# Kernel optimization log

Measured on AMD Instinct MI355X. Metric: run time of the kernel, lower is better.

The kernel has to match this reference:

```python
import jax, jax.numpy as jnp
import numpy as np

N = 50000      # nodes
E = 800000     # edges (before self loops)
IN, H, OUT = 128, 64, 64
NEG_SLOPE = 0.2  # PyG GATConv leaky_relu slope


def _glorot(k, shape):
    lim = float(np.sqrt(6.0 / (shape[0] + shape[1])))
    return jax.random.uniform(k, shape, jnp.float32, -lim, lim)


def setup_inputs() -> dict:
    key = jax.random.key(0)
    ks = jax.random.split(key, 16)
    x = jax.random.normal(ks[0], (N, IN), jnp.float32)
    edge_src = jax.random.randint(ks[1], (E,), 0, N, jnp.int32)
    edge_dst = jax.random.randint(ks[2], (E,), 0, N, jnp.int32)
    dims = [(IN, H), (H, H), (H, OUT)]
    inp = {"x": x, "edge_src": edge_src, "edge_dst": edge_dst}
    i = 3
    for l, (di, do) in enumerate(dims):
        inp[f"W{l}"] = _glorot(ks[i], (di, do)); i += 1
        inp[f"as{l}"] = _glorot(ks[i], (1, do))[0]; i += 1
        inp[f"ad{l}"] = _glorot(ks[i], (1, do))[0]; i += 1
        inp[f"b{l}"] = jnp.zeros((do,), jnp.float32)
    return inp


def _gat_layer(x, W, a_src, a_dst, b, src, dst):
    # single-head GATConv (PyG semantics, self loops already in src/dst)
    h = x @ W                              # [N, do]
    s = h @ a_src                          # [N] source attention logits
    d = h @ a_dst                          # [N] dest attention logits
    e = jax.nn.leaky_relu(s[src] + d[dst], NEG_SLOPE)   # [E']
    # segment softmax over incoming edges of each destination node
    m = jax.ops.segment_max(e, dst, num_segments=N)
    w = jnp.exp(e - m[dst])
    denom = jax.ops.segment_sum(w, dst, num_segments=N)
    coef = w / (denom[dst] + 1e-16)
    out = jax.ops.segment_sum(h[src] * coef[:, None], dst, num_segments=N)
    return out + b


def reference(x, edge_src, edge_dst, W0, as0, ad0, b0, W1, as1, ad1, b1, W2, as2, ad2, b2):
    # add self loops (GATConv default add_self_loops=True)
    loop = jnp.arange(N, dtype=edge_src.dtype)
    src = jnp.concatenate([edge_src, loop])
    dst = jnp.concatenate([edge_dst, loop])
    h = jax.nn.relu(_gat_layer(x, W0, as0, ad0, b0, src, dst))
    # dropout is identity in eval mode
    h = jax.nn.relu(_gat_layer(h, W1, as1, ad1, b1, src, dst))
    return _gat_layer(h, W2, as2, ad2, b2, src, dst)
```

## Files before the change

### kernel.cpp

```cpp
#include <hip/hip_runtime.h>
#include <hip/hip_fp16.h>
#include <math.h>

#define WAVE 64
#define NEG_SLOPE 0.2f
#define BCAP 4096
#define CSTR (BCAP + 128)

typedef _Float16 half8 __attribute__((ext_vector_type(8)));
typedef float f32x4 __attribute__((ext_vector_type(4)));


template <int K, int IS_HALF>
__device__ __forceinline__ void gemm_body(
    char* smemRaw, int t, int bid,
    const void* __restrict__ Xv, const float* __restrict__ W,
    const float* __restrict__ a_s, const float* __restrict__ a_d,
    __half* __restrict__ H, float* __restrict__ S, float* __restrict__ D,
    int n) {
    constexpr int AK = K + 8;
    _Float16* Xs = (_Float16*)smemRaw;
    _Float16* Bt = Xs + 64 * AK;
    int base = bid * 64;

    {
        int row = t >> 2, q = t & 3;
        int grow = base + row;
        constexpr int CW = K / 4;
        if constexpr (IS_HALF) {
            const __half* Xh = (const __half*)Xv;
#pragma unroll
            for (int c0 = 0; c0 < CW; c0 += 8) {
                uint4 v = make_uint4(0, 0, 0, 0);
                if (grow < n) v = *(const uint4*)(Xh + (size_t)grow * K + q * CW + c0);
                *(uint4*)(Xs + row * AK + q * CW + c0) = v;
            }
        } else {
            const float* X = (const float*)Xv;
#pragma unroll
            for (int c0 = 0; c0 < CW; c0 += 8) {
                float4 v0 = make_float4(0.f, 0.f, 0.f, 0.f), v1 = v0;
                if (grow < n) {
                    v0 = *(const float4*)(X + (size_t)grow * K + q * CW + c0);
                    v1 = *(const float4*)(X + (size_t)grow * K + q * CW + c0 + 4);
                }
                _Float16 h[8] = {(_Float16)v0.x, (_Float16)v0.y, (_Float16)v0.z, (_Float16)v0.w,
                                 (_Float16)v1.x, (_Float16)v1.y, (_Float16)v1.z, (_Float16)v1.w};
                *(uint4*)(Xs + row * AK + q * CW + c0) = *(uint4*)h;
            }
        }
    }
    {
        int nn = t & 63, g = t >> 6;
        constexpr int KW = K / 4;
        _Float16 hbuf[KW];
#pragma unroll
        for (int j = 0; j < KW; ++j)
            hbuf[j] = (_Float16)W[(size_t)(g * KW + j) * 64 + nn];
#pragma unroll
        for (int j = 0; j < KW; j += 8)
            *(uint4*)(Bt + nn * AK + g * KW + j) = *(uint4*)(hbuf + j);
    }
    __syncthreads();

    int lane = t & 63;
    int wv = t >> 6;
    int m0 = wv * 16;
    int l15 = lane & 15, quad = lane >> 4;

    f32x4 acc[4] = {{0.f, 0.f, 0.f, 0.f}, {0.f, 0.f, 0.f, 0.f},
                    {0.f, 0.f, 0.f, 0.f}, {0.f, 0.f, 0.f, 0.f}};
#pragma unroll
    for (int ks = 0; ks < K; ks += 32) {
        half8 a = *(half8*)(Xs + (m0 + l15) * AK + ks + quad * 8);
#pragma unroll
        for (int cg = 0; cg < 4; ++cg) {
            half8 b = *(half8*)(Bt + (cg * 16 + l15) * AK + ks + quad * 8);
            acc[cg] = __builtin_amdgcn_mfma_f32_16x16x32_f16(a, b, acc[cg], 0, 0, 0);
        }
    }

    float as_c[4], ad_c[4];
#pragma unroll
    for (int cg = 0; cg < 4; ++cg) {
        as_c[cg] = a_s[cg * 16 + l15];
        ad_c[cg] = a_d[cg * 16 + l15];
    }
#pragma unroll
    for (int r = 0; r < 4; ++r) {
        int grow = base + m0 + quad * 4 + r;
        bool ok = grow < n;
        float ps = 0.f, pd = 0.f;
#pragma unroll
        for (int cg = 0; cg < 4; ++cg) {
            float v = acc[cg][r];
            if (ok) H[(size_t)grow * 64 + cg * 16 + l15] = __float2half(v);
            ps += v * as_c[cg];
            pd += v * ad_c[cg];
        }
        for (int o = 1; o < 16; o <<= 1) {
            ps += __shfl_xor(ps, o);
            pd += __shfl_xor(pd, o);
        }
        if (l15 == 0 && ok) { S[grow] = ps; D[grow] = pd; }
    }
}

__global__ __launch_bounds__(256) void place_gemm0_kernel(
    const int* __restrict__ src, const int* __restrict__ dst,
    int* __restrict__ gfill, int* __restrict__ binned, int e, int nb, int nchunk,
    const float* __restrict__ X, const float* __restrict__ W,
    const float* __restrict__ a_s, const float* __restrict__ a_d,
    __half* __restrict__ H, float* __restrict__ S, float* __restrict__ D, int n) {
    extern __shared__ char smem[];
    if ((int)blockIdx.x >= nchunk) {
        gemm_body<128, 0>(smem, threadIdx.x, blockIdx.x - nchunk,
                          X, W, a_s, a_d, H, S, D, n);
        return;
    }
    int* cnt = (int*)smem;
    int* bas = cnt + nb;
    for (int b = threadIdx.x; b < nb; b += 256) cnt[b] = 0;
    __syncthreads();
    int base = blockIdx.x * 4096;
#pragma unroll
    for (int k = 0; k < 16; ++k) {
        int i = base + k * 256 + threadIdx.x;
        if (i < e) atomicAdd(&cnt[dst[i] >> 7], 1);
    }
    __syncthreads();
    for (int b = threadIdx.x; b < nb; b += 256) {
        int c = cnt[b];
        bas[b] = c ? atomicAdd(&gfill[b], c) : 0;
        cnt[b] = 0;
    }
    __syncthreads();
#pragma unroll
    for (int k = 0; k < 16; ++k) {
        int i = base + k * 256 + threadIdx.x;
        if (i < e) {
            int d = dst[i];
            int bk = d >> 7;
            int r = atomicAdd(&cnt[bk], 1);
            binned[(size_t)bk * BCAP + bas[bk] + r] = ((d & 127) << 16) | src[i];
        }
    }
}

__global__ __launch_bounds__(256) void bucket_build_kernel(
    const int* __restrict__ binned, const int* __restrict__ gfill,
    int* __restrict__ csr_src, int2* __restrict__ rowse, int n) {
    __shared__ int cnt[128], off[128], pcnt[128];
    int b = blockIdx.x;
    int t = threadIdx.x;
    int nodeBase = b << 7;
    int nc = min(128, n - nodeBase);
    int ne = min(gfill[b], BCAP);
    const int* bp = binned + (size_t)b * BCAP;
    if (t < 128) { cnt[t] = 1; pcnt[t] = 1; }
    __syncthreads();
    for (int i = t; i < ne; i += 256)
        atomicAdd(&cnt[bp[i] >> 16], 1);
    __syncthreads();
    if (t < 128) off[t] = cnt[t];
    __syncthreads();
    for (int o = 1; o < 128; o <<= 1) {
        int u = (t >= o && t < 128) ? off[t - o] : 0;
        __syncthreads();
        if (t < 128) off[t] += u;
        __syncthreads();
    }
    if (t < 128) off[t] -= cnt[t];
    __syncthreads();
    int csrBase = b * CSTR;
    if (t < nc) {
        int st = csrBase + off[t];
        rowse[nodeBase + t] = make_int2(st, st + cnt[t]);
        csr_src[st] = nodeBase + t;
    }
    for (int i = t; i < ne; i += 256) {
        int p = bp[i];
        int loc = p >> 16;
        int r = atomicAdd(&pcnt[loc], 1);
        csr_src[csrBase + off[loc] + r] = p & 0xFFFF;
    }
}

template <int K, int IS_HALF>
__global__ __launch_bounds__(256) void mfma_gemm_feat_kernel(
    const void* __restrict__ Xv, const float* __restrict__ W,
    const float* __restrict__ a_s, const float* __restrict__ a_d,
    __half* __restrict__ H, float* __restrict__ S, float* __restrict__ D, int n) {
    __shared__ char smem[2 * 64 * (K + 8) * 2];
    gemm_body<K, IS_HALF>(smem, threadIdx.x, blockIdx.x, Xv, W, a_s, a_d, H, S, D, n);
}


template <int WRITE_HALF>
__global__ __launch_bounds__(256) void gat_aggregate_kernel(
    const __half* __restrict__ H, const float* __restrict__ S,
    const float* __restrict__ D, const int2* __restrict__ rowse,
    const int* __restrict__ csr_src, const float* __restrict__ bias,
    void* __restrict__ OUTp, int n, int do_relu) {
    int wid  = (blockIdx.x * blockDim.x + threadIdx.x) >> 6;
    int lane = threadIdx.x & 63;
    if (wid >= n) return;
    int eg = lane >> 3;
    int cg = lane & 7;
    int2 se = rowse[wid];
    int start = se.x, end = se.y;
    float d_i = D[wid];

    float z = 0.f;
    float acc[8] = {0.f, 0.f, 0.f, 0.f, 0.f, 0.f, 0.f, 0.f};

    for (int cb = start; cb < end; cb += WAVE) {
        int j = cb + lane;
        bool v = j < end;
        int sc = v ? csr_src[j] : 0;
        float sv = S[sc];
        float e = sv + d_i;
        e = (e > 0.f) ? e : NEG_SLOPE * e;
        float w = v ? __expf(e) : 0.f;
        z += w;

        int nch = min(WAVE, end - cb);
        int rounds = (nch + 7) >> 3;
#pragma unroll 4
        for (int r = 0; r < rounds; ++r) {
            int idx = 8 * r + eg;
            float wr = __shfl(w, idx);
            int   sr = __shfl(sc, idx);
            if (idx < nch) {
                uint4 u = *(const uint4*)(H + (size_t)sr * 64 + 8 * cg);
                float2 f0 = __half22float2(*(__half2*)&u.x);
                float2 f1 = __half22float2(*(__half2*)&u.y);
                float2 f2 = __half22float2(*(__half2*)&u.z);
                float2 f3 = __half22float2(*(__half2*)&u.w);
                acc[0] = fmaf(wr, f0.x, acc[0]);
                acc[1] = fmaf(wr, f0.y, acc[1]);
                acc[2] = fmaf(wr, f1.x, acc[2]);
                acc[3] = fmaf(wr, f1.y, acc[3]);
                acc[4] = fmaf(wr, f2.x, acc[4]);
                acc[5] = fmaf(wr, f2.y, acc[5]);
                acc[6] = fmaf(wr, f3.x, acc[6]);
                acc[7] = fmaf(wr, f3.y, acc[7]);
            }
        }
    }

    z += __shfl_xor(z, 1);
    z += __shfl_xor(z, 2);
    z += __shfl_xor(z, 4);
    for (int o = 8; o < 64; o <<= 1) {
#pragma unroll
        for (int jj = 0; jj < 8; ++jj) acc[jj] += __shfl_xor(acc[jj], o);
        z += __shfl_xor(z, o);
    }

    if (eg == 0) {
        float inv = 1.f / (z + 1e-16f);
        const float4 bv0 = *(const float4*)(bias + 8 * cg);
        const float4 bv1 = *(const float4*)(bias + 8 * cg + 4);
        float o[8];
        o[0] = acc[0] * inv + bv0.x;
        o[1] = acc[1] * inv + bv0.y;
        o[2] = acc[2] * inv + bv0.z;
        o[3] = acc[3] * inv + bv0.w;
        o[4] = acc[4] * inv + bv1.x;
        o[5] = acc[5] * inv + bv1.y;
        o[6] = acc[6] * inv + bv1.z;
        o[7] = acc[7] * inv + bv1.w;
        if (do_relu) {
#pragma unroll
            for (int jj = 0; jj < 8; ++jj) o[jj] = fmaxf(o[jj], 0.f);
        }
        if constexpr (WRITE_HALF) {
            _Float16 h[8];
#pragma unroll
            for (int jj = 0; jj < 8; ++jj) h[jj] = (_Float16)o[jj];
            *(uint4*)((__half*)OUTp + (size_t)wid * 64 + 8 * cg) = *(uint4*)h;
        } else {
            float* OUT = (float*)OUTp;
            *(float4*)(OUT + (size_t)wid * 64 + 8 * cg) = make_float4(o[0], o[1], o[2], o[3]);
            *(float4*)(OUT + (size_t)wid * 64 + 8 * cg + 4) = make_float4(o[4], o[5], o[6], o[7]);
        }
    }
}


static inline size_t align256(size_t x) { return (x + 255) & ~(size_t)255; }

extern "C" void kernel_launch(void* const* d_in, const int* in_sizes, int n_in,
                              void* d_out, int out_size, void* d_ws, size_t ws_size,
                              hipStream_t stream) {
    const float* x    = (const float*)d_in[0];
    const int*   esrc = (const int*)d_in[1];
    const int*   edst = (const int*)d_in[2];
    const int E = in_sizes[1];
    const int N = in_sizes[0] / 128;

    const float* W0 = (const float*)d_in[3];
    const float* as0 = (const float*)d_in[4];
    const float* ad0 = (const float*)d_in[5];
    const float* b0 = (const float*)d_in[6];
    const float* W1 = (const float*)d_in[7];
    const float* as1 = (const float*)d_in[8];
    const float* ad1 = (const float*)d_in[9];
    const float* b1 = (const float*)d_in[10];
    const float* W2 = (const float*)d_in[11];
    const float* as2 = (const float*)d_in[12];
    const float* ad2 = (const float*)d_in[13];
    const float* b2 = (const float*)d_in[14];

    const int NB = (N + 127) >> 7;

    char* p = (char*)d_ws;
    int*  gfill   = (int*)p;  p += align256((size_t)(NB + 1) * 4);
    int2* rowse   = (int2*)p; p += align256((size_t)N * 8);
    int*  csr_src = (int*)p;  p += align256((size_t)NB * CSTR * 4);
    int*  binned  = (int*)p;  p += align256((size_t)NB * BCAP * 4);
    __half* h16 = (__half*)p; p += align256((size_t)N * 64 * 2);
    __half* hA  = (__half*)p; p += align256((size_t)N * 64 * 2);
    __half* hB  = (__half*)p; p += align256((size_t)N * 64 * 2);
    float* sA = (float*)p; p += align256((size_t)N * 4);
    float* dA = (float*)p; p += align256((size_t)N * 4);
    float* out = (float*)d_out;

    int nchunk = (E + 4095) / 4096;
    int tile_grid = (N + 63) / 64;
    int agg_grid  = (N + 3) / 4;

    hipMemsetAsync(gfill, 0, (size_t)(NB + 1) * 4, stream);

    place_gemm0_kernel<<<nchunk + tile_grid, 256, 34816, stream>>>(
        esrc, edst, gfill, binned, E, NB, nchunk,
        x, W0, as0, ad0, h16, sA, dA, N);

    bucket_build_kernel<<<NB, 256, 0, stream>>>(binned, gfill, csr_src, rowse, N);

    gat_aggregate_kernel<1><<<agg_grid, 256, 0, stream>>>(
        h16, sA, dA, rowse, csr_src, b0, hA, N, 1);

    mfma_gemm_feat_kernel<64, 1><<<tile_grid, 256, 0, stream>>>(hA, W1, as1, ad1, h16, sA, dA, N);
    gat_aggregate_kernel<1><<<agg_grid, 256, 0, stream>>>(
        h16, sA, dA, rowse, csr_src, b1, hB, N, 1);

    mfma_gemm_feat_kernel<64, 1><<<tile_grid, 256, 0, stream>>>(hB, W2, as2, ad2, h16, sA, dA, N);
    gat_aggregate_kernel<0><<<agg_grid, 256, 0, stream>>>(
        h16, sA, dA, rowse, csr_src, b2, out, N, 0);
}
```

Baseline: 235.0 us.

## Fuse GAT aggregation with next layer's MFMA feature GEMM

Replaces the separate aggregate and GEMM kernels for layers 0→1 and 1→2 with a single kernel. Each 512-thread block aggregates 64 nodes into shared memory as fp16, then runs the MFMA projection and the attention-logit reduction on that tile. This removes two kernel launches and the global write and read of the intermediate hidden activations, and adds ping-pong H/S/D buffers. It also widens bucket_build to 512 threads. The cost is that each wave now handles 8 nodes serially, which can lower latency hiding in the gather phase.

```diff
diff --git a/kernel.cpp b/kernel.cpp
--- a/kernel.cpp
+++ b/kernel.cpp
@@ -147,7 +147,7 @@
     }
 }
 
-__global__ __launch_bounds__(256) void bucket_build_kernel(
+__global__ __launch_bounds__(512) void bucket_build_kernel(
     const int* __restrict__ binned, const int* __restrict__ gfill,
     int* __restrict__ csr_src, int2* __restrict__ rowse, int n) {
     __shared__ int cnt[128], off[128], pcnt[128];
@@ -159,7 +159,7 @@
     const int* bp = binned + (size_t)b * BCAP;
     if (t < 128) { cnt[t] = 1; pcnt[t] = 1; }
     __syncthreads();
-    for (int i = t; i < ne; i += 256)
+    for (int i = t; i < ne; i += 512)
         atomicAdd(&cnt[bp[i] >> 16], 1);
     __syncthreads();
     if (t < 128) off[t] = cnt[t];
@@ -178,7 +178,7 @@
         rowse[nodeBase + t] = make_int2(st, st + cnt[t]);
         csr_src[st] = nodeBase + t;
     }
-    for (int i = t; i < ne; i += 256) {
+    for (int i = t; i < ne; i += 512) {
         int p = bp[i];
         int loc = p >> 16;
         int r = atomicAdd(&pcnt[loc], 1);
@@ -186,34 +186,19 @@
     }
 }
 
-template <int K, int IS_HALF>
-__global__ __launch_bounds__(256) void mfma_gemm_feat_kernel(
-    const void* __restrict__ Xv, const float* __restrict__ W,
-    const float* __restrict__ a_s, const float* __restrict__ a_d,
-    __half* __restrict__ H, float* __restrict__ S, float* __restrict__ D, int n) {
-    __shared__ char smem[2 * 64 * (K + 8) * 2];
-    gemm_body<K, IS_HALF>(smem, threadIdx.x, blockIdx.x, Xv, W, a_s, a_d, H, S, D, n);
-}
-
-
-template <int WRITE_HALF>
-__global__ __launch_bounds__(256) void gat_aggregate_kernel(
+
+__device__ __forceinline__ void agg_node(
     const __half* __restrict__ H, const float* __restrict__ S,
     const float* __restrict__ D, const int2* __restrict__ rowse,
-    const int* __restrict__ csr_src, const float* __restrict__ bias,
-    void* __restrict__ OUTp, int n, int do_relu) {
-    int wid  = (blockIdx.x * blockDim.x + threadIdx.x) >> 6;
-    int lane = threadIdx.x & 63;
+    const int* __restrict__ csr_src, int wid, int n, int lane, int eg, int cg,
+    float& z, float (&acc)[8]) {
+    z = 0.f;
+#pragma unroll
+    for (int jj = 0; jj < 8; ++jj) acc[jj] = 0.f;
     if (wid >= n) return;
-    int eg = lane >> 3;
-    int cg = lane & 7;
     int2 se = rowse[wid];
     int start = se.x, end = se.y;
     float d_i = D[wid];
-
-    float z = 0.f;
-    float acc[8] = {0.f, 0.f, 0.f, 0.f, 0.f, 0.f, 0.f, 0.f};
-
     for (int cb = start; cb < end; cb += WAVE) {
         int j = cb + lane;
         bool v = j < end;
@@ -223,7 +208,6 @@
         e = (e > 0.f) ? e : NEG_SLOPE * e;
         float w = v ? __expf(e) : 0.f;
         z += w;
-
         int nch = min(WAVE, end - cb);
         int rounds = (nch + 7) >> 3;
 #pragma unroll 4
@@ -248,7 +232,9 @@
             }
         }
     }
-
+}
+
+__device__ __forceinline__ void agg_reduce(float& z, float (&acc)[8]) {
     z += __shfl_xor(z, 1);
     z += __shfl_xor(z, 2);
     z += __shfl_xor(z, 4);
@@ -257,34 +243,126 @@
         for (int jj = 0; jj < 8; ++jj) acc[jj] += __shfl_xor(acc[jj], o);
         z += __shfl_xor(z, o);
     }
-
+}
+
+
+__global__ __launch_bounds__(512, 8) void agg_gemm_kernel(
+    const __half* __restrict__ H, const float* __restrict__ S,
+    const float* __restrict__ D, const int2* __restrict__ rowse,
+    const int* __restrict__ csr_src, const float* __restrict__ bias,
+    const float* __restrict__ W, const float* __restrict__ a_s,
+    const float* __restrict__ a_d, __half* __restrict__ Hout,
+    float* __restrict__ Sout, float* __restrict__ Dout, int n) {
+    constexpr int AK = 72;
+    __shared__ _Float16 Xs[64 * AK];
+    __shared__ _Float16 Bt[64 * AK];
+    __shared__ float Sb[64], Db[64];
+    int t = threadIdx.x;
+    int lane = t & 63;
+    int wv = t >> 6;
+    int base = blockIdx.x * 64;
+
+    {
+        _Float16 hbuf[8];
+#pragma unroll
+        for (int j = 0; j < 8; ++j)
+            hbuf[j] = (_Float16)W[(size_t)(wv * 8 + j) * 64 + lane];
+        *(uint4*)(Bt + lane * AK + wv * 8) = *(uint4*)hbuf;
+    }
+    if (t < 64) { Sb[t] = 0.f; Db[t] = 0.f; }
+
+    int eg = lane >> 3, cg = lane & 7;
+    const float4 bv0 = *(const float4*)(bias + 8 * cg);
+    const float4 bv1 = *(const float4*)(bias + 8 * cg + 4);
+    for (int i = 0; i < 8; ++i) {
+        int wid = base + wv * 8 + i;
+        float z, acc[8];
+        agg_node(H, S, D, rowse, csr_src, wid, n, lane, eg, cg, z, acc);
+        agg_reduce(z, acc);
+        if (eg == 0) {
+            float inv = 1.f / (z + 1e-16f);
+            float o[8];
+            o[0] = acc[0] * inv + bv0.x;
+            o[1] = acc[1] * inv + bv0.y;
+            o[2] = acc[2] * inv + bv0.z;
+            o[3] = acc[3] * inv + bv0.w;
+            o[4] = acc[4] * inv + bv1.x;
+            o[5] = acc[5] * inv + bv1.y;
+            o[6] = acc[6] * inv + bv1.z;
+            o[7] = acc[7] * inv + bv1.w;
+            _Float16 h[8];
+#pragma unroll
+            for (int jj = 0; jj < 8; ++jj) h[jj] = (_Float16)fmaxf(o[jj], 0.f);
+            *(uint4*)(Xs + (wv * 8 + i) * AK + 8 * cg) = *(uint4*)h;
+        }
+    }
+    __syncthreads();
+
+    int l15 = lane & 15, quad = lane >> 4;
+#pragma unroll
+    for (int k2 = 0; k2 < 2; ++k2) {
+        int tt = wv * 2 + k2;
+        int wr = tt & 3, wc = tt >> 2;
+        f32x4 a2 = {0.f, 0.f, 0.f, 0.f};
+#pragma unroll
+        for (int ks = 0; ks < 64; ks += 32) {
+            half8 a = *(half8*)(Xs + (wr * 16 + l15) * AK + ks + quad * 8);
+            half8 b = *(half8*)(Bt + (wc * 16 + l15) * AK + ks + quad * 8);
+            a2 = __builtin_amdgcn_mfma_f32_16x16x32_f16(a, b, a2, 0, 0, 0);
+        }
+        float asv = a_s[wc * 16 + l15], adv = a_d[wc * 16 + l15];
+#pragma unroll
+        for (int r = 0; r < 4; ++r) {
+            int row = wr * 16 + quad * 4 + r;
+            int grow = base + row;
+            float v = a2[r];
+            if (grow < n) Hout[(size_t)grow * 64 + wc * 16 + l15] = __float2half(v);
+            float ps = v * asv, pd = v * adv;
+            for (int o = 1; o < 16; o <<= 1) {
+                ps += __shfl_xor(ps, o);
+                pd += __shfl_xor(pd, o);
+            }
+            if (l15 == 0) {
+                atomicAdd(&Sb[row], ps);
+                atomicAdd(&Db[row], pd);
+            }
+        }
+    }
+    __syncthreads();
+    if (t < 64 && base + t < n) {
+        Sout[base + t] = Sb[t];
+        Dout[base + t] = Db[t];
+    }
+}
+
+
+__global__ __launch_bounds__(256) void gat_aggregate_final(
+    const __half* __restrict__ H, const float* __restrict__ S,
+    const float* __restrict__ D, const int2* __restrict__ rowse,
+    const int* __restrict__ csr_src, const float* __restrict__ bias,
+    float* __restrict__ OUT, int n) {
+    int wid  = (blockIdx.x * blockDim.x + threadIdx.x) >> 6;
+    int lane = threadIdx.x & 63;
+    if (wid >= n) return;
+    int eg = lane >> 3, cg = lane & 7;
+    float z, acc[8];
+    agg_node(H, S, D, rowse, csr_src, wid, n, lane, eg, cg, z, acc);
+    agg_reduce(z, acc);
     if (eg == 0) {
         float inv = 1.f / (z + 1e-16f);
         const float4 bv0 = *(const float4*)(bias + 8 * cg);
         const float4 bv1 = *(const float4*)(bias + 8 * cg + 4);
-        float o[8];
-        o[0] = acc[0] * inv + bv0.x;
-        o[1] = acc[1] * inv + bv0.y;
-        o[2] = acc[2] * inv + bv0.z;
-        o[3] = acc[3] * inv + bv0.w;
-        o[4] = acc[4] * inv + bv1.x;
-        o[5] = acc[5] * inv + bv1.y;
-        o[6] = acc[6] * inv + bv1.z;
-        o[7] = acc[7] * inv + bv1.w;
-        if (do_relu) {
-#pragma unroll
-            for (int jj = 0; jj < 8; ++jj) o[jj] = fmaxf(o[jj], 0.f);
-        }
-        if constexpr (WRITE_HALF) {
-            _Float16 h[8];
-#pragma unroll
-            for (int jj = 0; jj < 8; ++jj) h[jj] = (_Float16)o[jj];
-            *(uint4*)((__half*)OUTp + (size_t)wid * 64 + 8 * cg) = *(uint4*)h;
-        } else {
-            float* OUT = (float*)OUTp;
-            *(float4*)(OUT + (size_t)wid * 64 + 8 * cg) = make_float4(o[0], o[1], o[2], o[3]);
-            *(float4*)(OUT + (size_t)wid * 64 + 8 * cg + 4) = make_float4(o[4], o[5], o[6], o[7]);
-        }
+        float4 o0, o1;
+        o0.x = acc[0] * inv + bv0.x;
+        o0.y = acc[1] * inv + bv0.y;
+        o0.z = acc[2] * inv + bv0.z;
+        o0.w = acc[3] * inv + bv0.w;
+        o1.x = acc[4] * inv + bv1.x;
+        o1.y = acc[5] * inv + bv1.y;
+        o1.z = acc[6] * inv + bv1.z;
+        o1.w = acc[7] * inv + bv1.w;
+        *(float4*)(OUT + (size_t)wid * 64 + 8 * cg) = o0;
+        *(float4*)(OUT + (size_t)wid * 64 + 8 * cg + 4) = o1;
     }
 }
 
@@ -320,11 +398,12 @@
     int2* rowse   = (int2*)p; p += align256((size_t)N * 8);
     int*  csr_src = (int*)p;  p += align256((size_t)NB * CSTR * 4);
     int*  binned  = (int*)p;  p += align256((size_t)NB * BCAP * 4);
-    __half* h16 = (__half*)p; p += align256((size_t)N * 64 * 2);
-    __half* hA  = (__half*)p; p += align256((size_t)N * 64 * 2);
-    __half* hB  = (__half*)p; p += align256((size_t)N * 64 * 2);
+    __half* h16a = (__half*)p; p += align256((size_t)N * 64 * 2);
+    __half* h16b = (__half*)p; p += align256((size_t)N * 64 * 2);
     float* sA = (float*)p; p += align256((size_t)N * 4);
     float* dA = (float*)p; p += align256((size_t)N * 4);
+    float* sB = (float*)p; p += align256((size_t)N * 4);
+    float* dB = (float*)p; p += align256((size_t)N * 4);
     float* out = (float*)d_out;
 
     int nchunk = (E + 4095) / 4096;
@@ -335,18 +414,16 @@
 
     place_gemm0_kernel<<<nchunk + tile_grid, 256, 34816, stream>>>(
         esrc, edst, gfill, binned, E, NB, nchunk,
-        x, W0, as0, ad0, h16, sA, dA, N);
-
-    bucket_build_kernel<<<NB, 256, 0, stream>>>(binned, gfill, csr_src, rowse, N);
-
-    gat_aggregate_kernel<1><<<agg_grid, 256, 0, stream>>>(
-        h16, sA, dA, rowse, csr_src, b0, hA, N, 1);
-
-    mfma_gemm_feat_kernel<64, 1><<<tile_grid, 256, 0, stream>>>(hA, W1, as1, ad1, h16, sA, dA, N);
-    gat_aggregate_kernel<1><<<agg_grid, 256, 0, stream>>>(
-        h16, sA, dA, rowse, csr_src, b1, hB, N, 1);
-
-    mfma_gemm_feat_kernel<64, 1><<<tile_grid, 256, 0, stream>>>(hB, W2, as2, ad2, h16, sA, dA, N);
-    gat_aggregate_kernel<0><<<agg_grid, 256, 0, stream>>>(
-        h16, sA, dA, rowse, csr_src, b2, out, N, 0);
-}
+        x, W0, as0, ad0, h16a, sA, dA, N);
+
+    bucket_build_kernel<<<NB, 512, 0, stream>>>(binned, gfill, csr_src, rowse, N);
+
+    agg_gemm_kernel<<<tile_grid, 512, 0, stream>>>(
+        h16a, sA, dA, rowse, csr_src, b0, W1, as1, ad1, h16b, sB, dB, N);
+
+    agg_gemm_kernel<<<tile_grid, 512, 0, stream>>>(
+        h16b, sB, dB, rowse, csr_src, b1, W2, as2, ad2, h16a, sA, dA, N);
+
+    gat_aggregate_final<<<agg_grid, 256, 0, stream>>>(
+        h16a, sA, dA, rowse, csr_src, b2, out, N);
+}
```

New measurement: 238.9 us. About the same (+1.7%).

## Precompute per-edge attention weights into packed weight/source array before aggregation

Applied to the files above, without the earlier changes.

Edge attention weights exp(leaky_relu(S[src]+D[dst])) are now computed per edge in a separate pass, fused into bucket_build for layer 0 and done by a new weight_kernel for later layers. They are stored as packed (weight, src) pairs in CSR order. The aggregate kernel then reads these pairs directly and drops the S gather, the exp and the shuffle-broadcast stage. This trades an extra kernel launch and an 8-byte-per-edge write and read for a simpler, more latency-tolerant gather loop. The max subtraction is still absent, as before.

```diff
diff --git a/kernel.cpp b/kernel.cpp
--- a/kernel.cpp
+++ b/kernel.cpp
@@ -147,9 +147,11 @@
     }
 }
 
-__global__ __launch_bounds__(256) void bucket_build_kernel(
+__global__ __launch_bounds__(512) void bucket_build_kernel(
     const int* __restrict__ binned, const int* __restrict__ gfill,
-    int* __restrict__ csr_src, int2* __restrict__ rowse, int n) {
+    int* __restrict__ csr, int2* __restrict__ rowse,
+    const float* __restrict__ S, const float* __restrict__ D,
+    uint2* __restrict__ wsrc, int n) {
     __shared__ int cnt[128], off[128], pcnt[128];
     int b = blockIdx.x;
     int t = threadIdx.x;
@@ -159,7 +161,7 @@
     const int* bp = binned + (size_t)b * BCAP;
     if (t < 128) { cnt[t] = 1; pcnt[t] = 1; }
     __syncthreads();
-    for (int i = t; i < ne; i += 256)
+    for (int i = t; i < ne; i += 512)
         atomicAdd(&cnt[bp[i] >> 16], 1);
     __syncthreads();
     if (t < 128) off[t] = cnt[t];
@@ -176,13 +178,42 @@
     if (t < nc) {
         int st = csrBase + off[t];
         rowse[nodeBase + t] = make_int2(st, st + cnt[t]);
-        csr_src[st] = nodeBase + t;
-    }
-    for (int i = t; i < ne; i += 256) {
+        csr[st] = (t << 16) | (nodeBase + t);
+    }
+    for (int i = t; i < ne; i += 512) {
         int p = bp[i];
         int loc = p >> 16;
         int r = atomicAdd(&pcnt[loc], 1);
-        csr_src[csrBase + off[loc] + r] = p & 0xFFFF;
+        csr[csrBase + off[loc] + r] = p;
+    }
+    __syncthreads();
+    int total = nc + ne;
+    for (int i = t; i < total; i += 512) {
+        int p = csr[csrBase + i];
+        int sc = p & 0xFFFF;
+        float e = S[sc] + D[nodeBase + (p >> 16)];
+        e = (e > 0.f) ? e : NEG_SLOPE * e;
+        wsrc[csrBase + i] = make_uint2(__float_as_uint(__expf(e)), sc);
+    }
+}
+
+__global__ __launch_bounds__(256) void weight_kernel(
+    const int* __restrict__ csr, const float* __restrict__ S,
+    const float* __restrict__ D, const int* __restrict__ gfill,
+    uint2* __restrict__ wsrc, int n) {
+    int b = blockIdx.x >> 2;
+    int part = blockIdx.x & 3;
+    int nodeBase = b << 7;
+    int nc = min(128, n - nodeBase);
+    int ne = min(gfill[b], BCAP);
+    int csrBase = b * CSTR;
+    int total = nc + ne;
+    for (int i = part * 256 + threadIdx.x; i < total; i += 1024) {
+        int p = csr[csrBase + i];
+        int sc = p & 0xFFFF;
+        float e = S[sc] + D[nodeBase + (p >> 16)];
+        e = (e > 0.f) ? e : NEG_SLOPE * e;
+        wsrc[csrBase + i] = make_uint2(__float_as_uint(__expf(e)), sc);
     }
 }
 
@@ -198,9 +229,8 @@
 
 template <int WRITE_HALF>
 __global__ __launch_bounds__(256) void gat_aggregate_kernel(
-    const __half* __restrict__ H, const float* __restrict__ S,
-    const float* __restrict__ D, const int2* __restrict__ rowse,
-    const int* __restrict__ csr_src, const float* __restrict__ bias,
+    const __half* __restrict__ H, const uint2* __restrict__ wsrc,
+    const int2* __restrict__ rowse, const float* __restrict__ bias,
     void* __restrict__ OUTp, int n, int do_relu) {
     int wid  = (blockIdx.x * blockDim.x + threadIdx.x) >> 6;
     int lane = threadIdx.x & 63;
@@ -209,54 +239,42 @@
     int cg = lane & 7;
     int2 se = rowse[wid];
     int start = se.x, end = se.y;
-    float d_i = D[wid];
 
     float z = 0.f;
     float acc[8] = {0.f, 0.f, 0.f, 0.f, 0.f, 0.f, 0.f, 0.f};
 
-    for (int cb = start; cb < end; cb += WAVE) {
-        int j = cb + lane;
+    int R = (end - start + 7) >> 3;
+#pragma unroll 4
+    for (int r = 0; r < R; ++r) {
+        int j = start + 8 * r + eg;
         bool v = j < end;
-        int sc = v ? csr_src[j] : 0;
-        float sv = S[sc];
-        float e = sv + d_i;
-        e = (e > 0.f) ? e : NEG_SLOPE * e;
-        float w = v ? __expf(e) : 0.f;
-        z += w;
-
-        int nch = min(WAVE, end - cb);
-        int rounds = (nch + 7) >> 3;
-#pragma unroll 4
-        for (int r = 0; r < rounds; ++r) {
-            int idx = 8 * r + eg;
-            float wr = __shfl(w, idx);
-            int   sr = __shfl(sc, idx);
-            if (idx < nch) {
-                uint4 u = *(const uint4*)(H + (size_t)sr * 64 + 8 * cg);
-                float2 f0 = __half22float2(*(__half2*)&u.x);
-                float2 f1 = __half22float2(*(__half2*)&u.y);
-                float2 f2 = __half22float2(*(__half2*)&u.z);
-                float2 f3 = __half22float2(*(__half2*)&u.w);
-                acc[0] = fmaf(wr, f0.x, acc[0]);
-                acc[1] = fmaf(wr, f0.y, acc[1]);
-                acc[2] = fmaf(wr, f1.x, acc[2]);
-                acc[3] = fmaf(wr, f1.y, acc[3]);
-                acc[4] = fmaf(wr, f2.x, acc[4]);
-                acc[5] = fmaf(wr, f2.y, acc[5]);
-                acc[6] = fmaf(wr, f3.x, acc[6]);
-                acc[7] = fmaf(wr, f3.y, acc[7]);
-            }
-        }
-    }
-
-    z += __shfl_xor(z, 1);
-    z += __shfl_xor(z, 2);
-    z += __shfl_xor(z, 4);
+        uint2 ws = v ? wsrc[j] : make_uint2(0u, 0u);
+        float wr = v ? __uint_as_float(ws.x) : 0.f;
+        int   sr = ws.y;
+        if (v) {
+            uint4 u = *(const uint4*)(H + (size_t)sr * 64 + 8 * cg);
+            float2 f0 = __half22float2(*(__half2*)&u.x);
+            float2 f1 = __half22float2(*(__half2*)&u.y);
+            float2 f2 = __half22float2(*(__half2*)&u.z);
+            float2 f3 = __half22float2(*(__half2*)&u.w);
+            acc[0] = fmaf(wr, f0.x, acc[0]);
+            acc[1] = fmaf(wr, f0.y, acc[1]);
+            acc[2] = fmaf(wr, f1.x, acc[2]);
+            acc[3] = fmaf(wr, f1.y, acc[3]);
+            acc[4] = fmaf(wr, f2.x, acc[4]);
+            acc[5] = fmaf(wr, f2.y, acc[5]);
+            acc[6] = fmaf(wr, f3.x, acc[6]);
+            acc[7] = fmaf(wr, f3.y, acc[7]);
+        }
+        z += (cg == 0) ? wr : 0.f;
+    }
+
     for (int o = 8; o < 64; o <<= 1) {
 #pragma unroll
         for (int jj = 0; jj < 8; ++jj) acc[jj] += __shfl_xor(acc[jj], o);
         z += __shfl_xor(z, o);
     }
+    z = __shfl(z, 0);
 
     if (eg == 0) {
         float inv = 1.f / (z + 1e-16f);
@@ -318,13 +336,17 @@
     char* p = (char*)d_ws;
     int*  gfill   = (int*)p;  p += align256((size_t)(NB + 1) * 4);
     int2* rowse   = (int2*)p; p += align256((size_t)N * 8);
-    int*  csr_src = (int*)p;  p += align256((size_t)NB * CSTR * 4);
+    int*  csr     = (int*)p;  p += align256((size_t)NB * CSTR * 4);
     int*  binned  = (int*)p;  p += align256((size_t)NB * BCAP * 4);
-    __half* h16 = (__half*)p; p += align256((size_t)N * 64 * 2);
-    __half* hA  = (__half*)p; p += align256((size_t)N * 64 * 2);
-    __half* hB  = (__half*)p; p += align256((size_t)N * 64 * 2);
+    uint2* wsrc   = (uint2*)p; p += align256((size_t)NB * CSTR * 8);
+    __half* h16a = (__half*)p; p += align256((size_t)N * 64 * 2);
+    __half* h16b = (__half*)p; p += align256((size_t)N * 64 * 2);
+    __half* hA   = (__half*)p; p += align256((size_t)N * 64 * 2);
+    __half* hB   = (__half*)p; p += align256((size_t)N * 64 * 2);
     float* sA = (float*)p; p += align256((size_t)N * 4);
     float* dA = (float*)p; p += align256((size_t)N * 4);
+    float* sB = (float*)p; p += align256((size_t)N * 4);
+    float* dB = (float*)p; p += align256((size_t)N * 4);
     float* out = (float*)d_out;
 
     int nchunk = (E + 4095) / 4096;
@@ -335,18 +357,23 @@
 
     place_gemm0_kernel<<<nchunk + tile_grid, 256, 34816, stream>>>(
         esrc, edst, gfill, binned, E, NB, nchunk,
-        x, W0, as0, ad0, h16, sA, dA, N);
-
-    bucket_build_kernel<<<NB, 256, 0, stream>>>(binned, gfill, csr_src, rowse, N);
+        x, W0, as0, ad0, h16a, sA, dA, N);
+
+    bucket_build_kernel<<<NB, 512, 0, stream>>>(
+        binned, gfill, csr, rowse, sA, dA, wsrc, N);
 
     gat_aggregate_kernel<1><<<agg_grid, 256, 0, stream>>>(
-        h16, sA, dA, rowse, csr_src, b0, hA, N, 1);
-
-    mfma_gemm_feat_kernel<64, 1><<<tile_grid, 256, 0, stream>>>(hA, W1, as1, ad1, h16, sA, dA, N);
+        h16a, wsrc, rowse, b0, hA, N, 1);
+
+    mfma_gemm_feat_kernel<64, 1><<<tile_grid, 256, 0, stream>>>(
+        hA, W1, as1, ad1, h16b, sB, dB, N);
+    weight_kernel<<<NB * 4, 256, 0, stream>>>(csr, sB, dB, gfill, wsrc, N);
     gat_aggregate_kernel<1><<<agg_grid, 256, 0, stream>>>(
-        h16, sA, dA, rowse, csr_src, b1, hB, N, 1);
-
-    mfma_gemm_feat_kernel<64, 1><<<tile_grid, 256, 0, stream>>>(hB, W2, as2, ad2, h16, sA, dA, N);
+        h16b, wsrc, rowse, b1, hB, N, 1);
+
+    mfma_gemm_feat_kernel<64, 1><<<tile_grid, 256, 0, stream>>>(
+        hB, W2, as2, ad2, h16a, sA, dA, N);
+    weight_kernel<<<NB * 4, 256, 0, stream>>>(csr, sA, dA, gfill, wsrc, N);
     gat_aggregate_kernel<0><<<agg_grid, 256, 0, stream>>>(
-        h16, sA, dA, rowse, csr_src, b2, out, N, 0);
-}
+        h16a, wsrc, rowse, b2, out, N, 0);
+}
```

New measurement: 240.4 us. 1.02x slower.

## Replace binned CSR build with fixed-capacity per-node slot adjacency

Applied to the files above, without the earlier changes.

Removes the two-pass bucket binning and the separate bucket_build kernel. Each edge now atomically increments a per-node degree counter and writes its source into a fixed 128-slot row for its destination. The aggregation kernel reads the slots directly and adds the self loop implicitly. It also computes the softmax weights per edge group instead of through a wave-wide shuffle. This drops one kernel launch and one intermediate pass, at the cost of contended global atomics, a much larger slot buffer, and silently dropping edges past 128 in-degree.

```diff
diff --git a/kernel.cpp b/kernel.cpp
--- a/kernel.cpp
+++ b/kernel.cpp
@@ -4,8 +4,7 @@
 
 #define WAVE 64
 #define NEG_SLOPE 0.2f
-#define BCAP 4096
-#define CSTR (BCAP + 128)
+#define SCAP 128
 
 typedef _Float16 half8 __attribute__((ext_vector_type(8)));
 typedef float f32x4 __attribute__((ext_vector_type(4)));
@@ -108,7 +107,7 @@
 
 __global__ __launch_bounds__(256) void place_gemm0_kernel(
     const int* __restrict__ src, const int* __restrict__ dst,
-    int* __restrict__ gfill, int* __restrict__ binned, int e, int nb, int nchunk,
+    int* __restrict__ deg, int* __restrict__ slot, int e, int nchunk,
     const float* __restrict__ X, const float* __restrict__ W,
     const float* __restrict__ a_s, const float* __restrict__ a_d,
     __half* __restrict__ H, float* __restrict__ S, float* __restrict__ D, int n) {
@@ -118,71 +117,16 @@
                           X, W, a_s, a_d, H, S, D, n);
         return;
     }
-    int* cnt = (int*)smem;
-    int* bas = cnt + nb;
-    for (int b = threadIdx.x; b < nb; b += 256) cnt[b] = 0;
-    __syncthreads();
-    int base = blockIdx.x * 4096;
-#pragma unroll
-    for (int k = 0; k < 16; ++k) {
-        int i = base + k * 256 + threadIdx.x;
-        if (i < e) atomicAdd(&cnt[dst[i] >> 7], 1);
-    }
-    __syncthreads();
-    for (int b = threadIdx.x; b < nb; b += 256) {
-        int c = cnt[b];
-        bas[b] = c ? atomicAdd(&gfill[b], c) : 0;
-        cnt[b] = 0;
-    }
-    __syncthreads();
-#pragma unroll
-    for (int k = 0; k < 16; ++k) {
-        int i = base + k * 256 + threadIdx.x;
+    int base = blockIdx.x * 1024 + threadIdx.x;
+#pragma unroll
+    for (int k = 0; k < 4; ++k) {
+        int i = base + k * 256;
         if (i < e) {
             int d = dst[i];
-            int bk = d >> 7;
-            int r = atomicAdd(&cnt[bk], 1);
-            binned[(size_t)bk * BCAP + bas[bk] + r] = ((d & 127) << 16) | src[i];
-        }
-    }
-}
-
-__global__ __launch_bounds__(256) void bucket_build_kernel(
-    const int* __restrict__ binned, const int* __restrict__ gfill,
-    int* __restrict__ csr_src, int2* __restrict__ rowse, int n) {
-    __shared__ int cnt[128], off[128], pcnt[128];
-    int b = blockIdx.x;
-    int t = threadIdx.x;
-    int nodeBase = b << 7;
-    int nc = min(128, n - nodeBase);
-    int ne = min(gfill[b], BCAP);
-    const int* bp = binned + (size_t)b * BCAP;
-    if (t < 128) { cnt[t] = 1; pcnt[t] = 1; }
-    __syncthreads();
-    for (int i = t; i < ne; i += 256)
-        atomicAdd(&cnt[bp[i] >> 16], 1);
-    __syncthreads();
-    if (t < 128) off[t] = cnt[t];
-    __syncthreads();
-    for (int o = 1; o < 128; o <<= 1) {
-        int u = (t >= o && t < 128) ? off[t - o] : 0;
-        __syncthreads();
-        if (t < 128) off[t] += u;
-        __syncthreads();
-    }
-    if (t < 128) off[t] -= cnt[t];
-    __syncthreads();
-    int csrBase = b * CSTR;
-    if (t < nc) {
-        int st = csrBase + off[t];
-        rowse[nodeBase + t] = make_int2(st, st + cnt[t]);
-        csr_src[st] = nodeBase + t;
-    }
-    for (int i = t; i < ne; i += 256) {
-        int p = bp[i];
-        int loc = p >> 16;
-        int r = atomicAdd(&pcnt[loc], 1);
-        csr_src[csrBase + off[loc] + r] = p & 0xFFFF;
+            int s = src[i];
+            int r = atomicAdd(&deg[d], 1);
+            if (r < SCAP) slot[((size_t)d << 7) | r] = s;
+        }
     }
 }
 
@@ -199,64 +143,55 @@
 template <int WRITE_HALF>
 __global__ __launch_bounds__(256) void gat_aggregate_kernel(
     const __half* __restrict__ H, const float* __restrict__ S,
-    const float* __restrict__ D, const int2* __restrict__ rowse,
-    const int* __restrict__ csr_src, const float* __restrict__ bias,
+    const float* __restrict__ D, const int* __restrict__ deg,
+    const int* __restrict__ slot, const float* __restrict__ bias,
     void* __restrict__ OUTp, int n, int do_relu) {
     int wid  = (blockIdx.x * blockDim.x + threadIdx.x) >> 6;
     int lane = threadIdx.x & 63;
     if (wid >= n) return;
     int eg = lane >> 3;
     int cg = lane & 7;
-    int2 se = rowse[wid];
-    int start = se.x, end = se.y;
+    int dg = min(deg[wid], SCAP);
     float d_i = D[wid];
+    const int* srow = slot + ((size_t)wid << 7);
 
     float z = 0.f;
     float acc[8] = {0.f, 0.f, 0.f, 0.f, 0.f, 0.f, 0.f, 0.f};
 
-    for (int cb = start; cb < end; cb += WAVE) {
-        int j = cb + lane;
-        bool v = j < end;
-        int sc = v ? csr_src[j] : 0;
-        float sv = S[sc];
-        float e = sv + d_i;
-        e = (e > 0.f) ? e : NEG_SLOPE * e;
-        float w = v ? __expf(e) : 0.f;
-        z += w;
-
-        int nch = min(WAVE, end - cb);
-        int rounds = (nch + 7) >> 3;
-#pragma unroll 4
-        for (int r = 0; r < rounds; ++r) {
-            int idx = 8 * r + eg;
-            float wr = __shfl(w, idx);
-            int   sr = __shfl(sc, idx);
-            if (idx < nch) {
-                uint4 u = *(const uint4*)(H + (size_t)sr * 64 + 8 * cg);
-                float2 f0 = __half22float2(*(__half2*)&u.x);
-                float2 f1 = __half22float2(*(__half2*)&u.y);
-                float2 f2 = __half22float2(*(__half2*)&u.z);
-                float2 f3 = __half22float2(*(__half2*)&u.w);
-                acc[0] = fmaf(wr, f0.x, acc[0]);
-                acc[1] = fmaf(wr, f0.y, acc[1]);
-                acc[2] = fmaf(wr, f1.x, acc[2]);
-                acc[3] = fmaf(wr, f1.y, acc[3]);
-                acc[4] = fmaf(wr, f2.x, acc[4]);
-                acc[5] = fmaf(wr, f2.y, acc[5]);
-                acc[6] = fmaf(wr, f3.x, acc[6]);
-                acc[7] = fmaf(wr, f3.y, acc[7]);
-            }
-        }
-    }
-
-    z += __shfl_xor(z, 1);
-    z += __shfl_xor(z, 2);
-    z += __shfl_xor(z, 4);
+    int R = (dg + 1 + 7) >> 3;
+#pragma unroll 2
+    for (int r = 0; r < R; ++r) {
+        int idx = 8 * r + eg;
+        bool v = idx <= dg;
+        int sc = wid;
+        if (idx < dg) sc = srow[idx];
+        if (v) {
+            float e = S[sc] + d_i;
+            e = (e > 0.f) ? e : NEG_SLOPE * e;
+            float w = __expf(e);
+            uint4 u = *(const uint4*)(H + (size_t)sc * 64 + 8 * cg);
+            float2 f0 = __half22float2(*(__half2*)&u.x);
+            float2 f1 = __half22float2(*(__half2*)&u.y);
+            float2 f2 = __half22float2(*(__half2*)&u.z);
+            float2 f3 = __half22float2(*(__half2*)&u.w);
+            acc[0] = fmaf(w, f0.x, acc[0]);
+            acc[1] = fmaf(w, f0.y, acc[1]);
+            acc[2] = fmaf(w, f1.x, acc[2]);
+            acc[3] = fmaf(w, f1.y, acc[3]);
+            acc[4] = fmaf(w, f2.x, acc[4]);
+            acc[5] = fmaf(w, f2.y, acc[5]);
+            acc[6] = fmaf(w, f3.x, acc[6]);
+            acc[7] = fmaf(w, f3.y, acc[7]);
+            if (cg == 0) z += w;
+        }
+    }
+
     for (int o = 8; o < 64; o <<= 1) {
 #pragma unroll
         for (int jj = 0; jj < 8; ++jj) acc[jj] += __shfl_xor(acc[jj], o);
         z += __shfl_xor(z, o);
     }
+    z = __shfl(z, 0);
 
     if (eg == 0) {
         float inv = 1.f / (z + 1e-16f);
@@ -313,40 +248,39 @@
     const float* ad2 = (const float*)d_in[13];
     const float* b2 = (const float*)d_in[14];
 
-    const int NB = (N + 127) >> 7;
-
     char* p = (char*)d_ws;
-    int*  gfill   = (int*)p;  p += align256((size_t)(NB + 1) * 4);
-    int2* rowse   = (int2*)p; p += align256((size_t)N * 8);
-    int*  csr_src = (int*)p;  p += align256((size_t)NB * CSTR * 4);
-    int*  binned  = (int*)p;  p += align256((size_t)NB * BCAP * 4);
-    __half* h16 = (__half*)p; p += align256((size_t)N * 64 * 2);
-    __half* hA  = (__half*)p; p += align256((size_t)N * 64 * 2);
-    __half* hB  = (__half*)p; p += align256((size_t)N * 64 * 2);
+    int* deg  = (int*)p; p += align256((size_t)N * 4);
+    int* slot = (int*)p; p += align256((size_t)N * SCAP * 4);
+    __half* h16a = (__half*)p; p += align256((size_t)N * 64 * 2);
+    __half* h16b = (__half*)p; p += align256((size_t)N * 64 * 2);
+    __half* hA   = (__half*)p; p += align256((size_t)N * 64 * 2);
+    __half* hB   = (__half*)p; p += align256((size_t)N * 64 * 2);
     float* sA = (float*)p; p += align256((size_t)N * 4);
     float* dA = (float*)p; p += align256((size_t)N * 4);
+    float* sB = (float*)p; p += align256((size_t)N * 4);
+    float* dB = (float*)p; p += align256((size_t)N * 4);
     float* out = (float*)d_out;
 
-    int nchunk = (E + 4095) / 4096;
+    int nchunk = (E + 1023) / 1024;
     int tile_grid = (N + 63) / 64;
     int agg_grid  = (N + 3) / 4;
 
-    hipMemsetAsync(gfill, 0, (size_t)(NB + 1) * 4, stream);
+    hipMemsetAsync(deg, 0, (size_t)N * 4, stream);
 
     place_gemm0_kernel<<<nchunk + tile_grid, 256, 34816, stream>>>(
-        esrc, edst, gfill, binned, E, NB, nchunk,
-        x, W0, as0, ad0, h16, sA, dA, N);
-
-    bucket_build_kernel<<<NB, 256, 0, stream>>>(binned, gfill, csr_src, rowse, N);
+        esrc, edst, deg, slot, E, nchunk,
+        x, W0, as0, ad0, h16a, sA, dA, N);
 
     gat_aggregate_kernel<1><<<agg_grid, 256, 0, stream>>>(
-        h16, sA, dA, rowse, csr_src, b0, hA, N, 1);
-
-    mfma_gemm_feat_kernel<64, 1><<<tile_grid, 256, 0, stream>>>(hA, W1, as1, ad1, h16, sA, dA, N);
+        h16a, sA, dA, deg, slot, b0, hA, N, 1);
+
+    mfma_gemm_feat_kernel<64, 1><<<tile_grid, 256, 0, stream>>>(
+        hA, W1, as1, ad1, h16b, sB, dB, N);
     gat_aggregate_kernel<1><<<agg_grid, 256, 0, stream>>>(
-        h16, sA, dA, rowse, csr_src, b1, hB, N, 1);
-
-    mfma_gemm_feat_kernel<64, 1><<<tile_grid, 256, 0, stream>>>(hB, W2, as2, ad2, h16, sA, dA, N);
+        h16b, sB, dB, deg, slot, b1, hB, N, 1);
+
+    mfma_gemm_feat_kernel<64, 1><<<tile_grid, 256, 0, stream>>>(
+        hB, W2, as2, ad2, h16a, sA, dA, N);
     gat_aggregate_kernel<0><<<agg_grid, 256, 0, stream>>>(
-        h16, sA, dA, rowse, csr_src, b2, out, N, 0);
-}
+        h16a, sA, dA, deg, slot, b2, out, N, 0);
+}
```

New measurement: 263.8 us. 1.12x slower.
